# Kernel tuning notes

Hardware: AMD Instinct MI355X
Metric: run time of the kernel (lower is better)

The kernel has to match this reference:

```python
import jax, jax.numpy as jnp
import numpy as np

B, D, A = 512, 32, 10
NUM_CODES, CODE_DIM = 512, 64
COMMIT = 0.25


def _conv(x, w, b):
    # NHWC input, HWIO kernel, SAME padding, stride 1 (flax nn.Conv defaults)
    y = jax.lax.conv_general_dilated(x, w, (1, 1), 'SAME',
                                     dimension_numbers=('NHWC', 'HWIO', 'NHWC'))
    return y + b


def setup_inputs() -> dict:
    key = jax.random.key(0)
    ks = jax.random.split(key, 16)
    def rn(k, shape, scale):
        return jax.random.normal(k, shape, dtype=jnp.float32) * scale
    inp = {
        'x': rn(ks[0], (B, D, D), 1.0),
        'conv1_w': rn(ks[1], (3, 3, 1, 32), 0.3),
        'conv1_b': jnp.zeros((32,), jnp.float32),
        'conv2_w': rn(ks[2], (3, 3, 32, 64), 0.06),
        'conv2_b': jnp.zeros((64,), jnp.float32),
        'codebook': rn(ks[3], (NUM_CODES, CODE_DIM), 0.12),  # variance_scaling fan_in-ish
        'w1': rn(ks[4], (D * D * 64, 128), 0.004),
        'b1': jnp.zeros((128,), jnp.float32),
        'w2': rn(ks[5], (128, 128), 0.09),
        'b2': jnp.zeros((128,), jnp.float32),
        'w3': rn(ks[6], (128, 128), 0.09),
        'b3': jnp.zeros((128,), jnp.float32),
        'wa1': rn(ks[7], (128, 128), 0.09),
        'ba1': jnp.zeros((128,), jnp.float32),
        'wa2': rn(ks[8], (128, A), 0.09),
        'ba2': jnp.zeros((A,), jnp.float32),
        'wc1': rn(ks[9], (128, 128), 0.09),
        'bc1': jnp.zeros((128,), jnp.float32),
        'wc2': rn(ks[10], (128, 128), 0.09),
        'bc2': jnp.zeros((128,), jnp.float32),
        'wc3': rn(ks[11], (128, 1), 0.09),
        'bc3': jnp.zeros((1,), jnp.float32),
    }
    return inp


def reference(x, conv1_w, conv1_b, conv2_w, conv2_b, codebook,
              w1, b1, w2, b2, w3, b3,
              wa1, ba1, wa2, ba2,
              wc1, bc1, wc2, bc2, wc3, bc3):
    h = x.reshape(-1, D, D, 1)
    h = jax.nn.relu(_conv(h, conv1_w, conv1_b))
    h = jax.nn.relu(_conv(h, conv2_w, conv2_b))  # [B, D, D, 64]

    # --- Vector quantization (cdist + argmin + gather, straight-through) ---
    flat = h.reshape(-1, CODE_DIM)  # [B*D*D, 64]
    distances = (jnp.sum(flat ** 2, axis=1, keepdims=True)
                 - 2.0 * flat @ codebook.T
                 + jnp.sum(codebook ** 2, axis=1)[None, :])  # [N, num_codes]
    encoding_indices = jnp.argmin(distances, axis=1)
    quantized = codebook[encoding_indices].reshape(h.shape)
    quantized = h + jax.lax.stop_gradient(quantized - h)  # straight-through
    e_latent = jnp.mean((jax.lax.stop_gradient(quantized) - h) ** 2)
    q_latent = jnp.mean((quantized - jax.lax.stop_gradient(h)) ** 2)
    vq_loss = q_latent + COMMIT * e_latent

    # --- MLP trunk + actor-critic heads ---
    emb = quantized.reshape(quantized.shape[0], -1)
    emb = jax.nn.relu(emb @ w1 + b1)
    emb = jax.nn.relu(emb @ w2 + b2)
    emb = jax.nn.relu(emb @ w3 + b3)

    a = jax.nn.relu(emb @ wa1 + ba1)
    probs = jax.nn.softmax(a @ wa2 + ba2, axis=-1)  # Categorical probs

    c = jax.nn.relu(emb @ wc1 + bc1)
    c = jax.nn.relu(c @ wc2 + bc2)
    value = jnp.squeeze(c @ wc3 + bc3, axis=-1)

    return probs, value, vq_loss, encoding_indices
```

## Files before the change

kernel.cpp:

```cpp
#include <hip/hip_runtime.h>
#include <math.h>

#define NB 512
#define DD 32
#define NPX 1024
#define NTOT 524288
#define NC 512
#define CD 64

typedef float v2f __attribute__((ext_vector_type(2)));
typedef _Float16 hf;
typedef hf hf8 __attribute__((ext_vector_type(8)));
typedef float f32x4 __attribute__((ext_vector_type(4)));

__device__ __forceinline__ v2f pkfma(v2f a, v2f b, v2f c) {
    return __builtin_elementwise_fma(a, b, c);
}
__device__ __forceinline__ v2f splat2(float s) { v2f r; r.x = s; r.y = s; return r; }

__device__ __forceinline__ f32x4 mfma16(hf8 a, hf8 b, f32x4 c) {
    return __builtin_amdgcn_mfma_f32_16x16x32_f16(a, b, c, 0, 0, 0);
}

__device__ __forceinline__ float np_sumsq64(const float* a, int stride) {
    float r[8];
    #pragma unroll
    for (int j = 0; j < 8; ++j) {
        float v = a[j * stride];
        r[j] = __fmul_rn(v, v);
    }
    #pragma unroll
    for (int i = 1; i < 8; ++i)
        #pragma unroll
        for (int j = 0; j < 8; ++j) {
            float v = a[(i * 8 + j) * stride];
            r[j] = __fadd_rn(r[j], __fmul_rn(v, v));
        }
    return __fadd_rn(__fadd_rn(__fadd_rn(r[0], r[1]), __fadd_rn(r[2], r[3])),
                     __fadd_rn(__fadd_rn(r[4], r[5]), __fadd_rn(r[6], r[7])));
}

__global__ __launch_bounds__(256) void k_conv1(const float* __restrict__ x,
                                               const float* __restrict__ w,
                                               const float* __restrict__ bias,
                                               float* __restrict__ h1,
                                               const float* __restrict__ cb,
                                               const float* __restrict__ c2w,
                                               float* __restrict__ cnorm,
                                               hf* __restrict__ cbh,
                                               hf* __restrict__ cbl,
                                               hf* __restrict__ wTh,
                                               hf* __restrict__ wTl,
                                               float* __restrict__ accv) {
    const int b = blockIdx.x;
    const int tid = threadIdx.x;
    {
        int t = b * 256 + tid;
        if (t < NC)
            cnorm[t] = np_sumsq64(cb + (size_t)t * CD, 1);
        if (b < 128) {
            float a = cb[t] * 256.f;
            hf h0 = (hf)a;
            float rl = (a - (float)h0) * 2048.f;
            cbh[t] = h0;
            cbl[t] = (hf)rl;
        }
        if (b >= 128 && b < 200) {
            int t2 = (b - 128) * 256 + tid;
            if (t2 < 18432) {
                int s9 = t2 >> 11, rem = t2 & 2047;
                int co = rem >> 5, ci = rem & 31;
                float a = c2w[s9 * 2048 + ci * 64 + co] * 256.f;
                hf h0 = (hf)a;
                float rl = (a - (float)h0) * 2048.f;
                wTh[t2] = h0;
                wTl[t2] = (hf)rl;
            }
        }
        if (t == 0) accv[0] = 0.f;
    }
    __shared__ float xs[34][34];
    for (int i = tid; i < 34 * 34; i += 256) {
        int yy = i / 34, xx = i - yy * 34;
        float v = 0.f;
        if (yy >= 1 && yy <= 32 && xx >= 1 && xx <= 32)
            v = x[(size_t)b * NPX + (yy - 1) * 32 + (xx - 1)];
        xs[yy][xx] = v;
    }
    __syncthreads();
    for (int rep = 0; rep < 4; ++rep) {
        int px = tid + rep * 256;
        int y = px >> 5, xc = px & 31;
        v2f acc2[16];
        #pragma unroll
        for (int c = 0; c < 16; ++c) acc2[c] = splat2(0.f);
        #pragma unroll
        for (int dy = 0; dy < 3; ++dy)
        #pragma unroll
        for (int dx = 0; dx < 3; ++dx) {
            float a = xs[y + dy][xc + dx];
            v2f av = splat2(a);
            const v2f* wr = (const v2f*)(w + (dy * 3 + dx) * 32);
            #pragma unroll
            for (int c = 0; c < 16; ++c) acc2[c] = pkfma(av, wr[c], acc2[c]);
        }
        float4* out = (float4*)(h1 + ((size_t)b * NPX + px) * 32);
        #pragma unroll
        for (int q = 0; q < 8; ++q) {
            float4 v;
            v.x = fmaxf(__fadd_rn(acc2[q*2+0].x, bias[q*4+0]), 0.f);
            v.y = fmaxf(__fadd_rn(acc2[q*2+0].y, bias[q*4+1]), 0.f);
            v.z = fmaxf(__fadd_rn(acc2[q*2+1].x, bias[q*4+2]), 0.f);
            v.w = fmaxf(__fadd_rn(acc2[q*2+1].y, bias[q*4+3]), 0.f);
            out[q] = v;
        }
    }
}

#define CI_P 40
__global__ __launch_bounds__(512, 4) void k_conv2(const float* __restrict__ h1,
                                                  const hf* __restrict__ wTh,
                                                  const hf* __restrict__ wTl,
                                                  const float* __restrict__ bias,
                                                  float* __restrict__ h) {
    __shared__ hf Ah[10 * 34 * CI_P];
    __shared__ hf Al[10 * 34 * CI_P];
    const int blk = blockIdx.x;
    const int b = blk >> 2, strip = blk & 3;
    const int r0 = strip * 8;
    const int tid = threadIdx.x;
    for (int i = tid; i < 640; i += 512) {
        int ci = i & 31, rem = i >> 5;
        int ry = rem >> 1, colx = (rem & 1) * 33;
        int idx = (ry * 34 + colx) * CI_P + ci;
        Ah[idx] = (hf)0.f;
        Al[idx] = (hf)0.f;
    }
    #pragma unroll
    for (int r = 0; r < 5; ++r) {
        int j = tid + r * 512;
        int ci4 = j & 7, xc = (j >> 3) & 31, ry = j >> 8;
        int gy = r0 - 1 + ry;
        float4 v = make_float4(0.f, 0.f, 0.f, 0.f);
        if (gy >= 0 && gy < 32)
            v = *(const float4*)(h1 + ((size_t)b * NPX + gy * 32 + xc) * 32 + ci4 * 4);
        int bi = (ry * 34 + xc + 1) * CI_P + ci4 * 4;
        float fv[4] = {v.x, v.y, v.z, v.w};
        #pragma unroll
        for (int q = 0; q < 4; ++q) {
            float a = fv[q] * 256.f;
            hf h0 = (hf)a;
            float rl = (a - (float)h0) * 2048.f;
            Ah[bi + q] = h0;
            Al[bi + q] = (hf)rl;
        }
    }
    __syncthreads();
    const int w = tid >> 6, l = tid & 63;
    const int i16 = l & 15, j4 = l >> 4;
    #pragma unroll 1
    for (int ntp = 0; ntp < 2; ++ntp) {
        f32x4 hi[2][2], mid[2][2], llt[2][2];
        #pragma unroll
        for (int s = 0; s < 2; ++s)
            #pragma unroll
            for (int n = 0; n < 2; ++n) {
                hi[s][n] = f32x4{0.f, 0.f, 0.f, 0.f};
                mid[s][n] = f32x4{0.f, 0.f, 0.f, 0.f};
                llt[s][n] = f32x4{0.f, 0.f, 0.f, 0.f};
            }
        #pragma unroll 1
        for (int s9 = 0; s9 < 9; ++s9) {
            const int dy = s9 / 3, dx = s9 - dy * 3;
            hf8 a_h[2], a_l[2];
            #pragma unroll
            for (int s = 0; s < 2; ++s) {
                int ofs = ((w + dy) * 34 + (s * 16 + i16 + dx)) * CI_P + 8 * j4;
                a_h[s] = *(const hf8*)(Ah + ofs);
                a_l[s] = *(const hf8*)(Al + ofs);
            }
            #pragma unroll
            for (int ntl = 0; ntl < 2; ++ntl) {
                const int nt = ntp * 2 + ntl;
                const int wofs = (s9 * 64 + nt * 16 + i16) * 32 + 8 * j4;
                const hf8 b_h = *(const hf8*)(wTh + wofs);
                const hf8 b_l = *(const hf8*)(wTl + wofs);
                #pragma unroll
                for (int s = 0; s < 2; ++s) {
                    hi[s][ntl]  = mfma16(a_h[s], b_h, hi[s][ntl]);
                    mid[s][ntl] = mfma16(a_h[s], b_l, mid[s][ntl]);
                    mid[s][ntl] = mfma16(a_l[s], b_h, mid[s][ntl]);
                    llt[s][ntl] = mfma16(a_l[s], b_l, llt[s][ntl]);
                }
            }
        }
        #pragma unroll
        for (int ntl = 0; ntl < 2; ++ntl) {
            const int co = (ntp * 2 + ntl) * 16 + i16;
            const float bco = bias[co];
            #pragma unroll
            for (int s = 0; s < 2; ++s) {
                #pragma unroll
                for (int r = 0; r < 4; ++r) {
                    float comb = fmaf(mid[s][ntl][r], 4.8828125e-4f,
                                 fmaf(llt[s][ntl][r], 2.384185791015625e-7f,
                                      hi[s][ntl][r]));
                    float hv = fmaxf(
                        __fadd_rn(__fmul_rn(comb, 1.52587890625e-5f), bco), 0.f);
                    int px = w * 32 + s * 16 + j4 * 4 + r;
                    h[((size_t)b * NPX + r0 * 32 + px) * 64 + co] = hv;
                }
            }
        }
    }
}

#define TAU 2e-4f
__global__ __launch_bounds__(512, 4) void k_vq(const float* __restrict__ h,
                                               const float* __restrict__ h1,
                                               const float* __restrict__ c2w,
                                               const float* __restrict__ c2b,
                                               const float* __restrict__ cb,
                                               const hf* __restrict__ cbh,
                                               const hf* __restrict__ cbl,
                                               const float* __restrict__ cnorm,
                                               int* __restrict__ idxout,
                                               float* __restrict__ fidx,
                                               float* __restrict__ lossacc) {
    __shared__ float4 Ats[16][256];
    __shared__ float cn_lds[512];
    __shared__ int   mis_lds[256];
    __shared__ int   rlist[256];
    __shared__ float hex[8][64];
    __shared__ int   rcnt;
    const int tid = threadIdx.x;
    const size_t base = (size_t)blockIdx.x * 256;
    if (tid == 0) rcnt = 0;
    {
        const int px = tid & 255, half = tid >> 8;
        const float4* src = (const float4*)(h + (base + px) * 64 + half * 32);
        #pragma unroll
        for (int j = 0; j < 8; ++j)
            Ats[half * 8 + j][px] = src[j];
    }
    cn_lds[tid] = cnorm[tid];
    __syncthreads();
    const int w = tid >> 6, l = tid & 63;
    const int co = l & 15, g = l >> 4;
    const int pxw = w * 32;
    hf8 ah[2][2], al[2][2];
    #pragma unroll
    for (int s = 0; s < 2; ++s)
        #pragma unroll
        for (int ks = 0; ks < 2; ++ks) {
            float4 q0 = Ats[ks * 8 + g * 2 + 0][pxw + s * 16 + co];
            float4 q1 = Ats[ks * 8 + g * 2 + 1][pxw + s * 16 + co];
            float fv[8] = {q0.x, q0.y, q0.z, q0.w, q1.x, q1.y, q1.z, q1.w};
            #pragma unroll
            for (int j = 0; j < 8; ++j) {
                float fa = fv[j] * 256.f;
                hf h0 = (hf)fa;
                float rl = (fa - (float)h0) * 2048.f;
                ah[s][ks][j] = h0;
                al[s][ks][j] = (hf)rl;
            }
        }
    float minv[2][4], min2[2][4];
    int   mini[2][4];
    #pragma unroll
    for (int s = 0; s < 2; ++s)
        #pragma unroll
        for (int r = 0; r < 4; ++r) {
            minv[s][r] = 3.4e38f; min2[s][r] = 3.4e38f; mini[s][r] = 0;
        }
    const hf* pbh = cbh + (size_t)co * 64 + g * 8;
    const hf* pbl = cbl + (size_t)co * 64 + g * 8;
    #pragma unroll 1
    for (int t = 0; t < 32; ++t) {
        const hf8 bh0 = *(const hf8*)(pbh + (size_t)t * 1024);
        const hf8 bh1 = *(const hf8*)(pbh + (size_t)t * 1024 + 32);
        const hf8 bl0 = *(const hf8*)(pbl + (size_t)t * 1024);
        const hf8 bl1 = *(const hf8*)(pbl + (size_t)t * 1024 + 32);
        const float cn = cn_lds[t * 16 + co];
        #pragma unroll
        for (int s = 0; s < 2; ++s) {
            f32x4 hi = {0.f, 0.f, 0.f, 0.f};
            f32x4 lo = {0.f, 0.f, 0.f, 0.f};
            f32x4 ll = {0.f, 0.f, 0.f, 0.f};
            lo = mfma16(ah[s][0], bl0, lo);
            lo = mfma16(al[s][0], bh0, lo);
            ll = mfma16(al[s][0], bl0, ll);
            hi = mfma16(ah[s][0], bh0, hi);
            lo = mfma16(ah[s][1], bl1, lo);
            lo = mfma16(al[s][1], bh1, lo);
            ll = mfma16(al[s][1], bl1, ll);
            hi = mfma16(ah[s][1], bh1, hi);
            #pragma unroll
            for (int r = 0; r < 4; ++r) {
                float comb = fmaf(lo[r], 4.8828125e-4f,
                             fmaf(ll[r], 2.384185791015625e-7f, hi[r]));
                float d = __fsub_rn(cn, __fmul_rn(3.0517578125e-5f, comb));
                if (d < minv[s][r]) {
                    min2[s][r] = minv[s][r];
                    minv[s][r] = d; mini[s][r] = t * 16 + co;
                } else if (d < min2[s][r]) {
                    min2[s][r] = d;
                }
            }
        }
    }
    #pragma unroll
    for (int s = 0; s < 2; ++s)
        #pragma unroll
        for (int r = 0; r < 4; ++r) {
            float v1 = minv[s][r], v2 = min2[s][r];
            int i1 = mini[s][r];
            #pragma unroll
            for (int off = 1; off < 16; off <<= 1) {
                float vo  = __shfl_xor(v1, off, 64);
                int   io  = __shfl_xor(i1, off, 64);
                float v2o = __shfl_xor(v2, off, 64);
                if (vo < v1 || (vo == v1 && io < i1)) {
                    v2 = fminf(v1, v2o);
                    v1 = vo; i1 = io;
                } else {
                    v2 = fminf(v2, vo);
                }
            }
            if (co == 0) {
                int pxo = pxw + s * 16 + g * 4 + r;
                mis_lds[pxo] = i1;
                if (v2 - v1 <= TAU) {
                    int slot = atomicAdd(&rcnt, 1);
                    rlist[slot] = pxo;
                }
            }
        }
    __syncthreads();
    const int nresc = rcnt;
    for (int rr = w; rr < nresc; rr += 8) {
        const int px = rlist[rr];
        const int gpx = (int)base + px;
        const int bimg = gpx >> 10, pp = gpx & 1023;
        const int py = pp >> 5, pxx = pp & 31;
        float* hx = &hex[w][0];
        {
            float acc = 0.f;
            #pragma unroll 1
            for (int s9 = 0; s9 < 9; ++s9) {
                const int dy = s9 / 3, dx = s9 - dy * 3;
                const int gy = py + dy - 1, gx = pxx + dx - 1;
                if (gy >= 0 && gy < 32 && gx >= 0 && gx < 32) {
                    const float* hp = h1 + ((size_t)bimg * NPX + gy * 32 + gx) * 32;
                    const float* wp = c2w + s9 * 2048 + l;
                    #pragma unroll
                    for (int ci = 0; ci < 32; ++ci)
                        acc = fmaf(hp[ci], wp[ci * 64], acc);
                }
            }
            hx[l] = fmaxf(__fadd_rn(acc, c2b[l]), 0.f);
        }
        const float Hp = np_sumsq64(hx, 1);
        float bv = 3.4e38f; int bi2 = 0;
        const float* crow = cb + (size_t)(l * 8) * 64;
        #pragma unroll 1
        for (int c = 0; c < 8; ++c) {
            float acc0 = 0.f;
            const float* cr = crow + c * 64;
            #pragma unroll
            for (int kg = 0; kg < 16; ++kg) {
                acc0 = fmaf(hx[kg*4+0], cr[kg*4+0], acc0);
                acc0 = fmaf(hx[kg*4+1], cr[kg*4+1], acc0);
                acc0 = fmaf(hx[kg*4+2], cr[kg*4+2], acc0);
                acc0 = fmaf(hx[kg*4+3], cr[kg*4+3], acc0);
            }
            float d = __fadd_rn(__fsub_rn(Hp, __fmul_rn(2.f, acc0)),
                                cn_lds[l * 8 + c]);
            if (d < bv) { bv = d; bi2 = l * 8 + c; }
        }
        #pragma unroll
        for (int off = 1; off < 64; off <<= 1) {
            float vo = __shfl_xor(bv, off, 64);
            int   io = __shfl_xor(bi2, off, 64);
            if (vo < bv || (vo == bv && io < bi2)) { bv = vo; bi2 = io; }
        }
        if (l == 0) mis_lds[px] = bi2;
    }
    __syncthreads();
    if (tid < 256) {
        int bi = mis_lds[tid];
        idxout[base + tid] = bi;
        fidx[base + tid] = (float)bi;
        float ls = 0.f;
        const float* crow = cb + (size_t)bi * 64;
        #pragma unroll
        for (int kg = 0; kg < 16; ++kg) {
            float4 a = Ats[kg][tid];
            float d0 = crow[kg*4+0] - a.x;
            float d1 = crow[kg*4+1] - a.y;
            float d2 = crow[kg*4+2] - a.z;
            float d3 = crow[kg*4+3] - a.w;
            ls = fmaf(d0, d0, ls); ls = fmaf(d1, d1, ls);
            ls = fmaf(d2, d2, ls); ls = fmaf(d3, d3, ls);
        }
        #pragma unroll
        for (int off = 32; off > 0; off >>= 1)
            ls += __shfl_down(ls, off, 64);
        if ((tid & 63) == 0) atomicAdd(lossacc, ls);
    }
}

__global__ __launch_bounds__(256) void k_prepw1(const float* __restrict__ w1,
                                                hf* __restrict__ w1h,
                                                hf* __restrict__ w1l) {
    int t = blockIdx.x * 256 + threadIdx.x;
    int n = t & 127, k8 = t >> 7;
    hf vh[8], vl[8];
    #pragma unroll
    for (int j = 0; j < 8; ++j) {
        float a = w1[(size_t)(k8 * 8 + j) * 128 + n] * 256.f;
        hf h0 = (hf)a;
        float rl = (a - (float)h0) * 2048.f;
        vh[j] = h0;
        vl[j] = (hf)rl;
    }
    *(hf8*)(w1h + (size_t)k8 * 1024 + n * 8) = *(hf8*)vh;
    *(hf8*)(w1l + (size_t)k8 * 1024 + n * 8) = *(hf8*)vl;
}

__global__ __launch_bounds__(256) void k_fc1(const int* __restrict__ idxw,
                                             const hf* __restrict__ cbh,
                                             const hf* __restrict__ cbl,
                                             const hf* __restrict__ w1h,
                                             const hf* __restrict__ w1l,
                                             float* __restrict__ part) {
    const int kchunk = blockIdx.x;
    const int mtile  = blockIdx.y;
    const int tid = threadIdx.x;
    const int w = tid >> 6, l = tid & 63;
    const int co = l & 15, g = l >> 4;
    const int mbase = mtile * 64 + w * 16;
    f32x4 hi[8], mid[8];
    #pragma unroll
    for (int n = 0; n < 8; ++n) {
        hi[n] = f32x4{0.f, 0.f, 0.f, 0.f};
        mid[n] = f32x4{0.f, 0.f, 0.f, 0.f};
    }
    int code = 0;
    #pragma unroll 1
    for (int kstep = 0; kstep < 32; ++kstep) {
        if ((kstep & 1) == 0) {
            const int pix = kchunk * 16 + (kstep >> 1);
            code = idxw[(size_t)(mbase + co) * NPX + pix];
        }
        const int koff = (kstep & 1) * 32 + g * 8;
        const hf8 ah = *(const hf8*)(cbh + ((size_t)code << 6) + koff);
        const hf8 al = *(const hf8*)(cbl + ((size_t)code << 6) + koff);
        const size_t k8b = (size_t)(kchunk * 128 + kstep * 4 + g) * 1024;
        #pragma unroll
        for (int n = 0; n < 8; ++n) {
            const hf8 bh = *(const hf8*)(w1h + k8b + (n * 16 + co) * 8);
            const hf8 bl = *(const hf8*)(w1l + k8b + (n * 16 + co) * 8);
            hi[n]  = mfma16(ah, bh, hi[n]);
            mid[n] = mfma16(ah, bl, mid[n]);
            mid[n] = mfma16(al, bh, mid[n]);
        }
    }
    #pragma unroll
    for (int n = 0; n < 8; ++n)
        #pragma unroll
        for (int r = 0; r < 4; ++r) {
            float comb = fmaf(mid[n][r], 4.8828125e-4f, hi[n][r]);
            const int img = mtile * 64 + w * 16 + g * 4 + r;
            part[((size_t)kchunk * 512 + img) * 128 + n * 16 + co] =
                __fmul_rn(comb, 1.52587890625e-5f);
        }
}

__global__ __launch_bounds__(256) void k_reduce(const float* __restrict__ part,
                                                const float* __restrict__ b1,
                                                float* __restrict__ x0) {
    int t = blockIdx.x * 256 + threadIdx.x;
    float s = b1[t & 127];
    for (int ch = 0; ch < 64; ++ch)
        s += part[(size_t)ch * 65536 + t];
    x0[t] = fmaxf(s, 0.f);
}

__device__ __forceinline__ void mlp_layer(const float in[][16], float out[][16],
                                          const float* __restrict__ W,
                                          const float* __restrict__ bias,
                                          int tid, bool dorelu) {
    const int lane = tid & 63, wv = tid >> 6;
    const int img = lane & 15, cg = lane >> 4;
    const int c0 = wv * 32 + cg * 8;
    float acc[8] = {0,0,0,0,0,0,0,0};
    for (int k = 0; k < 128; ++k) {
        float a = in[k][img];
        float4 wA = *(const float4*)(W + (size_t)k * 128 + c0);
        float4 wB = *(const float4*)(W + (size_t)k * 128 + c0 + 4);
        acc[0] = fmaf(a, wA.x, acc[0]);
        acc[1] = fmaf(a, wA.y, acc[1]);
        acc[2] = fmaf(a, wA.z, acc[2]);
        acc[3] = fmaf(a, wA.w, acc[3]);
        acc[4] = fmaf(a, wB.x, acc[4]);
        acc[5] = fmaf(a, wB.y, acc[5]);
        acc[6] = fmaf(a, wB.z, acc[6]);
        acc[7] = fmaf(a, wB.w, acc[7]);
    }
    #pragma unroll
    for (int c = 0; c < 8; ++c) {
        float v = acc[c] + bias[c0 + c];
        if (dorelu) v = fmaxf(v, 0.f);
        out[c0 + c][img] = v;
    }
}

__global__ __launch_bounds__(256) void k_trunk(const float* __restrict__ x0,
        const float* __restrict__ w2, const float* __restrict__ b2,
        const float* __restrict__ w3, const float* __restrict__ b3,
        const float* __restrict__ wa1, const float* __restrict__ ba1,
        const float* __restrict__ wa2, const float* __restrict__ ba2,
        const float* __restrict__ wc1, const float* __restrict__ bc1,
        const float* __restrict__ wc2, const float* __restrict__ bc2,
        const float* __restrict__ wc3, const float* __restrict__ bc3,
        float* __restrict__ probs, float* __restrict__ value,
        const float* __restrict__ accv, float* __restrict__ vqloss) {
    __shared__ float bufA[128][16], bufB[128][16], bufC[128][16];
    __shared__ float lg[16][10];
    const int tid = threadIdx.x;
    const int m0 = blockIdx.x * 16;
    if (blockIdx.x == 0 && tid == 0)
        vqloss[0] = accv[0] * 1.25f / 33554432.f;
    for (int r = 0; r < 2; ++r) {
        int j = tid + r * 256;
        int img = j >> 5, k4 = j & 31;
        float4 v = *(const float4*)(x0 + (size_t)(m0 + img) * 128 + k4 * 4);
        bufA[k4*4+0][img] = v.x;
        bufA[k4*4+1][img] = v.y;
        bufA[k4*4+2][img] = v.z;
        bufA[k4*4+3][img] = v.w;
    }
    __syncthreads();
    mlp_layer(bufA, bufB, w2, b2, tid, true);   __syncthreads();
    mlp_layer(bufB, bufC, w3, b3, tid, true);   __syncthreads();
    mlp_layer(bufC, bufA, wa1, ba1, tid, true); __syncthreads();
    if (tid < 160) {
        int img = tid & 15, col = tid >> 4;
        float s = 0.f;
        for (int k = 0; k < 128; ++k)
            s = fmaf(bufA[k][img], wa2[(size_t)k * 10 + col], s);
        lg[img][col] = s + ba2[col];
    }
    __syncthreads();
    if (tid < 16) {
        int img = tid;
        float m = lg[img][0];
        #pragma unroll
        for (int c = 1; c < 10; ++c) m = fmaxf(m, lg[img][c]);
        float e[10]; float s = 0.f;
        #pragma unroll
        for (int c = 0; c < 10; ++c) { e[c] = expf(lg[img][c] - m); s += e[c]; }
        float inv = 1.f / s;
        #pragma unroll
        for (int c = 0; c < 10; ++c)
            probs[(size_t)(m0 + img) * 10 + c] = e[c] * inv;
    }
    __syncthreads();
    mlp_layer(bufC, bufB, wc1, bc1, tid, true); __syncthreads();
    mlp_layer(bufB, bufA, wc2, bc2, tid, true); __syncthreads();
    if (tid < 16) {
        int img = tid;
        float s = 0.f;
        for (int k = 0; k < 128; ++k)
            s = fmaf(bufA[k][img], wc3[k], s);
        value[m0 + img] = s + bc3[0];
    }
}

extern "C" void kernel_launch(void* const* d_in, const int* in_sizes, int n_in,
                              void* d_out, int out_size, void* d_ws, size_t ws_size,
                              hipStream_t stream) {
    const float* x   = (const float*)d_in[0];
    const float* c1w = (const float*)d_in[1];
    const float* c1b = (const float*)d_in[2];
    const float* c2w = (const float*)d_in[3];
    const float* c2b = (const float*)d_in[4];
    const float* cb  = (const float*)d_in[5];
    const float* w1  = (const float*)d_in[6];
    const float* b1  = (const float*)d_in[7];
    const float* w2  = (const float*)d_in[8];
    const float* b2  = (const float*)d_in[9];
    const float* w3  = (const float*)d_in[10];
    const float* b3  = (const float*)d_in[11];
    const float* wa1 = (const float*)d_in[12];
    const float* ba1 = (const float*)d_in[13];
    const float* wa2 = (const float*)d_in[14];
    const float* ba2 = (const float*)d_in[15];
    const float* wc1 = (const float*)d_in[16];
    const float* bc1 = (const float*)d_in[17];
    const float* wc2 = (const float*)d_in[18];
    const float* bc2 = (const float*)d_in[19];
    const float* wc3 = (const float*)d_in[20];
    const float* bc3 = (const float*)d_in[21];

    float* out = (float*)d_out;
    float* ws  = (float*)d_ws;

    float* h1    = ws;
    float* part  = ws;
    float* x0    = ws + (size_t)4 * 1024 * 1024;
    float* h     = ws + (size_t)16 * 1024 * 1024;
    hf*    w1Th  = (hf*)(ws + (size_t)16777216);
    hf*    w1Tl  = (hf*)(ws + (size_t)20971520);
    int*   idxw  = (int*)(ws + (size_t)50331648);
    float* cn    = ws + (size_t)50855936;
    float* accv  = ws + (size_t)50856448;
    hf*    cbh   = (hf*)(ws + (size_t)50857984);
    hf*    cbl   = (hf*)(ws + (size_t)50874368);
    hf*    wTh   = (hf*)(ws + (size_t)50890752);
    hf*    wTl   = (hf*)(ws + (size_t)50899968);

    hipLaunchKernelGGL(k_conv1,  dim3(512),   dim3(256), 0, stream, x, c1w, c1b, h1,
                       cb, c2w, cn, cbh, cbl, wTh, wTl, accv);
    hipLaunchKernelGGL(k_conv2,  dim3(2048),  dim3(512), 0, stream, h1, wTh, wTl,
                       c2b, h);
    hipLaunchKernelGGL(k_vq,     dim3(2048),  dim3(512), 0, stream, h, h1, c2w, c2b,
                       cb, cbh, cbl, cn, idxw, out + 5633, accv);
    hipLaunchKernelGGL(k_prepw1, dim3(4096),  dim3(256), 0, stream, w1, w1Th, w1Tl);
    hipLaunchKernelGGL(k_fc1,    dim3(64, 8), dim3(256), 0, stream, idxw, cbh, cbl,
                       w1Th, w1Tl, part);
    hipLaunchKernelGGL(k_reduce, dim3(256),   dim3(256), 0, stream, part, b1, x0);
    hipLaunchKernelGGL(k_trunk,  dim3(32),    dim3(256), 0, stream, x0,
                       w2, b2, w3, b3, wa1, ba1, wa2, ba2,
                       wc1, bc1, wc2, bc2, wc3, bc3,
                       out, out + 5120, accv, out + 5632);
}
```

Before: 710.7 us.

## Fuse conv2 into VQ kernel via shared memory and fold w1 prep into conv1

Merges the conv2 and vector-quantization kernels so conv2 outputs are written straight into the shared-memory tile the VQ stage reads, instead of round-tripping the 128MB activation tensor through global memory. The w1 split-fp16 conversion is moved into otherwise idle blocks of conv1, which removes a separate launch. The fused kernel uses more shared memory and its occupancy hint drops from 4 to 2 blocks per unit, and the conv1 blocks that do the w1 conversion now each loop over 16 rows.

```diff
diff --git a/kernel.cpp b/kernel.cpp
--- a/kernel.cpp
+++ b/kernel.cpp
@@ -46,11 +46,14 @@
                                                float* __restrict__ h1,
                                                const float* __restrict__ cb,
                                                const float* __restrict__ c2w,
+                                               const float* __restrict__ w1,
                                                float* __restrict__ cnorm,
                                                hf* __restrict__ cbh,
                                                hf* __restrict__ cbl,
                                                hf* __restrict__ wTh,
                                                hf* __restrict__ wTl,
+                                               hf* __restrict__ w1h,
+                                               hf* __restrict__ w1l,
                                                float* __restrict__ accv) {
     const int b = blockIdx.x;
     const int tid = threadIdx.x;
@@ -77,6 +80,25 @@
                 wTl[t2] = (hf)rl;
             }
         }
+        if (b >= 200 && b < 456) {
+            int t3 = (b - 200) * 256 + tid;
+            int n = t3 & 127;
+            int k8b = (t3 >> 7) * 16;
+            for (int kk = 0; kk < 16; ++kk) {
+                int k8 = k8b + kk;
+                hf vh[8], vl[8];
+                #pragma unroll
+                for (int j = 0; j < 8; ++j) {
+                    float a = w1[(size_t)(k8 * 8 + j) * 128 + n] * 256.f;
+                    hf h0 = (hf)a;
+                    float rl = (a - (float)h0) * 2048.f;
+                    vh[j] = h0;
+                    vl[j] = (hf)rl;
+                }
+                *(hf8*)(w1h + (size_t)k8 * 1024 + n * 8) = *(hf8*)vh;
+                *(hf8*)(w1l + (size_t)k8 * 1024 + n * 8) = *(hf8*)vl;
+            }
+        }
         if (t == 0) accv[0] = 0.f;
     }
     __shared__ float xs[34][34];
@@ -118,17 +140,34 @@
 }
 
 #define CI_P 40
-__global__ __launch_bounds__(512, 4) void k_conv2(const float* __restrict__ h1,
-                                                  const hf* __restrict__ wTh,
-                                                  const hf* __restrict__ wTl,
-                                                  const float* __restrict__ bias,
-                                                  float* __restrict__ h) {
+#define TAU 2e-4f
+__global__ __launch_bounds__(512, 2) void k_cvq(const float* __restrict__ h1,
+                                                const hf* __restrict__ wTh,
+                                                const hf* __restrict__ wTl,
+                                                const float* __restrict__ c2w,
+                                                const float* __restrict__ c2b,
+                                                const float* __restrict__ cb,
+                                                const hf* __restrict__ cbh,
+                                                const hf* __restrict__ cbl,
+                                                const float* __restrict__ cnorm,
+                                                int* __restrict__ idxout,
+                                                float* __restrict__ fidx,
+                                                float* __restrict__ lossacc) {
     __shared__ hf Ah[10 * 34 * CI_P];
     __shared__ hf Al[10 * 34 * CI_P];
+    __shared__ float4 Ats[16][256];
+    __shared__ float cn_lds[512];
+    __shared__ int   mis_lds[256];
+    __shared__ int   rlist[256];
+    __shared__ float hex[8][64];
+    __shared__ int   rcnt;
     const int blk = blockIdx.x;
     const int b = blk >> 2, strip = blk & 3;
     const int r0 = strip * 8;
     const int tid = threadIdx.x;
+    const size_t base = (size_t)blk * 256;
+    if (tid == 0) rcnt = 0;
+    cn_lds[tid] = cnorm[tid];
     for (int i = tid; i < 640; i += 512) {
         int ci = i & 31, rem = i >> 5;
         int ry = rem >> 1, colx = (rem & 1) * 33;
@@ -157,7 +196,7 @@
     }
     __syncthreads();
     const int w = tid >> 6, l = tid & 63;
-    const int i16 = l & 15, j4 = l >> 4;
+    const int co16 = l & 15, g = l >> 4;
     #pragma unroll 1
     for (int ntp = 0; ntp < 2; ++ntp) {
         f32x4 hi[2][2], mid[2][2], llt[2][2];
@@ -175,14 +214,14 @@
             hf8 a_h[2], a_l[2];
             #pragma unroll
             for (int s = 0; s < 2; ++s) {
-                int ofs = ((w + dy) * 34 + (s * 16 + i16 + dx)) * CI_P + 8 * j4;
+                int ofs = ((w + dy) * 34 + (s * 16 + co16 + dx)) * CI_P + 8 * g;
                 a_h[s] = *(const hf8*)(Ah + ofs);
                 a_l[s] = *(const hf8*)(Al + ofs);
             }
             #pragma unroll
             for (int ntl = 0; ntl < 2; ++ntl) {
                 const int nt = ntp * 2 + ntl;
-                const int wofs = (s9 * 64 + nt * 16 + i16) * 32 + 8 * j4;
+                const int wofs = (s9 * 64 + nt * 16 + co16) * 32 + 8 * g;
                 const hf8 b_h = *(const hf8*)(wTh + wofs);
                 const hf8 b_l = *(const hf8*)(wTl + wofs);
                 #pragma unroll
@@ -196,8 +235,8 @@
         }
         #pragma unroll
         for (int ntl = 0; ntl < 2; ++ntl) {
-            const int co = (ntp * 2 + ntl) * 16 + i16;
-            const float bco = bias[co];
+            const int co = (ntp * 2 + ntl) * 16 + co16;
+            const float bco = c2b[co];
             #pragma unroll
             for (int s = 0; s < 2; ++s) {
                 #pragma unroll
@@ -207,46 +246,14 @@
                                       hi[s][ntl][r]));
                     float hv = fmaxf(
                         __fadd_rn(__fmul_rn(comb, 1.52587890625e-5f), bco), 0.f);
-                    int px = w * 32 + s * 16 + j4 * 4 + r;
-                    h[((size_t)b * NPX + r0 * 32 + px) * 64 + co] = hv;
+                    int pxl = w * 32 + s * 16 + g * 4 + r;
+                    ((float*)&Ats[co >> 2][pxl])[co & 3] = hv;
                 }
             }
         }
     }
-}
-
-#define TAU 2e-4f
-__global__ __launch_bounds__(512, 4) void k_vq(const float* __restrict__ h,
-                                               const float* __restrict__ h1,
-                                               const float* __restrict__ c2w,
-                                               const float* __restrict__ c2b,
-                                               const float* __restrict__ cb,
-                                               const hf* __restrict__ cbh,
-                                               const hf* __restrict__ cbl,
-                                               const float* __restrict__ cnorm,
-                                               int* __restrict__ idxout,
-                                               float* __restrict__ fidx,
-                                               float* __restrict__ lossacc) {
-    __shared__ float4 Ats[16][256];
-    __shared__ float cn_lds[512];
-    __shared__ int   mis_lds[256];
-    __shared__ int   rlist[256];
-    __shared__ float hex[8][64];
-    __shared__ int   rcnt;
-    const int tid = threadIdx.x;
-    const size_t base = (size_t)blockIdx.x * 256;
-    if (tid == 0) rcnt = 0;
-    {
-        const int px = tid & 255, half = tid >> 8;
-        const float4* src = (const float4*)(h + (base + px) * 64 + half * 32);
-        #pragma unroll
-        for (int j = 0; j < 8; ++j)
-            Ats[half * 8 + j][px] = src[j];
-    }
-    cn_lds[tid] = cnorm[tid];
-    __syncthreads();
-    const int w = tid >> 6, l = tid & 63;
-    const int co = l & 15, g = l >> 4;
+    __syncthreads();
+    const int co = co16;
     const int pxw = w * 32;
     hf8 ah[2][2], al[2][2];
     #pragma unroll
@@ -408,24 +415,6 @@
             ls += __shfl_down(ls, off, 64);
         if ((tid & 63) == 0) atomicAdd(lossacc, ls);
     }
-}
-
-__global__ __launch_bounds__(256) void k_prepw1(const float* __restrict__ w1,
-                                                hf* __restrict__ w1h,
-                                                hf* __restrict__ w1l) {
-    int t = blockIdx.x * 256 + threadIdx.x;
-    int n = t & 127, k8 = t >> 7;
-    hf vh[8], vl[8];
-    #pragma unroll
-    for (int j = 0; j < 8; ++j) {
-        float a = w1[(size_t)(k8 * 8 + j) * 128 + n] * 256.f;
-        hf h0 = (hf)a;
-        float rl = (a - (float)h0) * 2048.f;
-        vh[j] = h0;
-        vl[j] = (hf)rl;
-    }
-    *(hf8*)(w1h + (size_t)k8 * 1024 + n * 8) = *(hf8*)vh;
-    *(hf8*)(w1l + (size_t)k8 * 1024 + n * 8) = *(hf8*)vl;
 }
 
 __global__ __launch_bounds__(256) void k_fc1(const int* __restrict__ idxw,
@@ -610,7 +599,6 @@
     float* h1    = ws;
     float* part  = ws;
     float* x0    = ws + (size_t)4 * 1024 * 1024;
-    float* h     = ws + (size_t)16 * 1024 * 1024;
     hf*    w1Th  = (hf*)(ws + (size_t)16777216);
     hf*    w1Tl  = (hf*)(ws + (size_t)20971520);
     int*   idxw  = (int*)(ws + (size_t)50331648);
@@ -622,12 +610,9 @@
     hf*    wTl   = (hf*)(ws + (size_t)50899968);
 
     hipLaunchKernelGGL(k_conv1,  dim3(512),   dim3(256), 0, stream, x, c1w, c1b, h1,
-                       cb, c2w, cn, cbh, cbl, wTh, wTl, accv);
-    hipLaunchKernelGGL(k_conv2,  dim3(2048),  dim3(512), 0, stream, h1, wTh, wTl,
-                       c2b, h);
-    hipLaunchKernelGGL(k_vq,     dim3(2048),  dim3(512), 0, stream, h, h1, c2w, c2b,
-                       cb, cbh, cbl, cn, idxw, out + 5633, accv);
-    hipLaunchKernelGGL(k_prepw1, dim3(4096),  dim3(256), 0, stream, w1, w1Th, w1Tl);
+                       cb, c2w, w1, cn, cbh, cbl, wTh, wTl, w1Th, w1Tl, accv);
+    hipLaunchKernelGGL(k_cvq,    dim3(2048),  dim3(512), 0, stream, h1, wTh, wTl,
+                       c2w, c2b, cb, cbh, cbl, cn, idxw, out + 5633, accv);
     hipLaunchKernelGGL(k_fc1,    dim3(64, 8), dim3(256), 0, stream, idxw, cbh, cbl,
                        w1Th, w1Tl, part);
     hipLaunchKernelGGL(k_reduce, dim3(256),   dim3(256), 0, stream, part, b1, x0);
```

New measurement: 710.5 us. Within noise of the previous version (-0.0%).
